# Kernel tuning notes

Hardware: AMD Instinct MI355X
Metric: run time of the kernel (lower is better)

Reference implementation:

```python
import jax, jax.numpy as jnp
import numpy as np

# dims
B, Nt, Ln, Lv = 16, 64, 256, 4      # batch, trees/batch, nodes/tree, value tokens/node
D = 256                              # embedding_dim
VOCAB, NTYPE = 32000, 64
M, Ls = 128, 4                       # story memory slots, tokens per slot
HOPS = 3                             # max_hops
COMP_STEP = 4                        # max tree depth = max(kb_n_layers)
LEVELS = [0, 1, 16, 64, 160, Ln]     # node index ranges per depth 0..4


def setup_inputs() -> dict:
    rng = np.random.default_rng(0)
    key = jax.random.key(0)
    ks = jax.random.split(key, 12)

    # --- tree structure: depth per node, father index in previous level ---
    depth = np.zeros(Ln, np.int64)
    father = np.zeros((B, Nt, Ln), np.int64)
    for lvl in range(1, 5):
        lo, hi = LEVELS[lvl], LEVELS[lvl + 1]
        depth[lo:hi] = lvl
        father[..., lo:hi] = rng.integers(LEVELS[lvl - 1], LEVELS[lvl], (B, Nt, hi - lo))
    father[..., 0] = Ln  # root's father = pad slot (torch -1 wraps to last index)
    kb_fathers = np.concatenate([father, np.full((B, Nt, 1), Ln, np.int64)], -1)  # [B,Nt,Ln+1]
    nl = np.broadcast_to(depth, (B, Nt, Ln))
    kb_n_layers = np.concatenate([nl, np.full((B, Nt, 1), -1, np.int64)], -1)     # [B,Nt,Ln+1]

    kb_values = rng.integers(1, VOCAB, (B, Nt, Ln, Lv))
    kb_types = rng.integers(1, NTYPE, (B, Nt, Ln))
    story = rng.integers(1, VOCAB, (B, M, Ls))
    decoder_input = rng.integers(1, VOCAB, (B,))

    s = 1.0 / np.sqrt(D)
    C = 0.1 * jax.random.normal(ks[0], (HOPS + 1, VOCAB, D), jnp.float32)
    C = C.at[:, 0].set(0.0)  # padding_idx = 0
    T_emb = 0.1 * jax.random.normal(ks[1], (NTYPE, D), jnp.float32)
    T_emb = T_emb.at[0].set(0.0)
    return {
        'decoder_input': jnp.asarray(decoder_input),
        'story': jnp.asarray(story),
        'hidden': 0.1 * jax.random.normal(ks[2], (1, B, D), jnp.float32),
        'kb_values': jnp.asarray(kb_values),
        'kb_types': jnp.asarray(kb_types),
        'kb_fathers': jnp.asarray(kb_fathers),
        'kb_n_layers': jnp.asarray(kb_n_layers),
        'C': C,
        'T_emb': T_emb,
        'Wq': s * jax.random.normal(ks[3], (D, D), jnp.float32),
        'Wk': s * jax.random.normal(ks[4], (D, D), jnp.float32),
        'Wv': s * jax.random.normal(ks[5], (D, D), jnp.float32),
        'W1_w': s * jax.random.normal(ks[6], (VOCAB, 2 * D), jnp.float32),
        'W1_b': jnp.zeros((VOCAB,), jnp.float32),
        'W_ih': s * jax.random.normal(ks[7], (3 * D, D), jnp.float32),
        'W_hh': s * jax.random.normal(ks[8], (3 * D, D), jnp.float32),
        'b_ih': jnp.zeros((3 * D,), jnp.float32),
        'b_hh': jnp.zeros((3 * D,), jnp.float32),
    }


def _forward(decoder_input, story, hidden, kb_values, kb_types, kb_fathers, kb_n_layers,
             C, T_emb, Wq, Wk, Wv, W1_w, W1_b, W_ih, W_hh, b_ih, b_hh):
    C0 = C[0]
    # ensemble: node embed = type_embed * sum(value token embeds)   [B,Nt,Ln,D]
    node = T_emb[kb_types] * C0[kb_values].sum(-2)
    node = jnp.concatenate([node, jnp.zeros((B, Nt, 1, D), node.dtype)], axis=2)  # pad slot
    nl = COMP_STEP - 1 - kb_n_layers  # adjusted layer counter
    base = jnp.arange(B * Nt).reshape(B, Nt, 1) * (Ln + 1)
    seg = (base + kb_fathers).reshape(-1)  # flat father ids for scatter-add

    def body(i, carry):
        node, nl = carry
        nxt = jax.ops.segment_sum(node.reshape(-1, D), seg,
                                  num_segments=B * Nt * (Ln + 1)).reshape(B, Nt, Ln + 1, D)
        node = node + nxt * (nl == 0)[..., None].astype(node.dtype)
        return (node, nl - 1)

    node, _ = jax.lax.fori_loop(0, COMP_STEP, body, (node, nl))
    roots = node[:, :, 0]                                   # [B,Nt,D]
    bias = jnp.where(roots.sum(-1) == 0, -1e9, 0.0)         # attention_bias [B,Nt]

    # compute_global_ranking: QKV attention over tree roots
    h = hidden[-1]                                          # [B,D]
    w = jax.nn.softmax(jnp.einsum('bnd,bd->bn', roots @ Wk.T, h @ Wq.T) + bias, axis=1)
    feat = jnp.einsum('bn,bnd->bd', w, roots @ Wv.T)        # kb_attn_features

    # single GRU step (PyTorch gate order r,z,n)
    x = C0[decoder_input]
    gi = x @ W_ih.T + b_ih
    gh = h @ W_hh.T + b_hh
    ir, iz, inn = jnp.split(gi, 3, -1)
    hr, hz, hn = jnp.split(gh, 3, -1)
    r = jax.nn.sigmoid(ir + hr)
    z = jax.nn.sigmoid(iz + hz)
    n = jnp.tanh(inn + r * hn)
    h_new = (1.0 - z) * n + z * h
    u = h_new + feat                                        # cur_state

    # ptrMemDecoder (Mem2Seq-style hops over story memory)
    p_vocab = None
    logits = None
    for hop in range(HOPS):
        m_A = C[hop][story].sum(2)                          # [B,M,D]
        logits = jnp.einsum('bmd,bd->bm', m_A, u)
        prob = jax.nn.softmax(logits, axis=1)
        m_C = C[hop + 1][story].sum(2)
        o = jnp.einsum('bm,bmd->bd', prob, m_C)
        if hop == 0:
            p_vocab = jnp.concatenate([u, o], -1) @ W1_w.T + W1_b
        u = u + o
    p_ptr = logits
    return p_ptr, p_vocab, h_new


def reference(decoder_input, story, hidden, kb_values, kb_types, kb_fathers, kb_n_layers,
              C, T_emb, Wq, Wk, Wv, W1_w, W1_b, W_ih, W_hh, b_ih, b_hh):
    return _forward(decoder_input, story, hidden, kb_values, kb_types, kb_fathers, kb_n_layers,
                    C, T_emb, Wq, Wk, Wv, W1_w, W1_b, W_ih, W_hh, b_ih, b_hh)
```

## Files before the change

### kernel.cpp

```cpp
#include <hip/hip_runtime.h>
#include <hip/hip_bf16.h>
#include <math.h>

#define B_ 16
#define NT 64
#define LN 256
#define LV 4
#define D_ 256
#define VOCAB_ 32000
#define M_ 128
#define LS 4
#define ECAP 192

typedef unsigned short ushort_t;
typedef unsigned int uint_t;

__device__ __forceinline__ ushort_t f2bf(float f) {
  uint_t u = __float_as_uint(f);
  uint_t r = u + 0x7FFFu + ((u >> 16) & 1u);
  return (ushort_t)(r >> 16);
}
__device__ __forceinline__ float bflo(uint_t u) {
  return __uint_as_float(u << 16);
}
__device__ __forceinline__ float bfhi(uint_t u) {
  return __uint_as_float(u & 0xFFFF0000u);
}

#define NB_S (3 * B_ * M_)
#define NB_CONV 2048
#define NB_TR 192
#define NB_TQK 256
#define NB_WVT 64
#define NB_BKT (B_ * NT)
__global__ __launch_bounds__(256) void k_prep(
    const int* __restrict__ story, const float* __restrict__ C,
    const float* __restrict__ W_ih, const float* __restrict__ W_hh,
    const float* __restrict__ Wq, const float* __restrict__ Wk,
    const float* __restrict__ Wv, const int* __restrict__ kb_values,
    const int* __restrict__ kb_types, float* __restrict__ S,
    ushort_t* __restrict__ C0h, float* __restrict__ W_ihT,
    float* __restrict__ W_hhT, float* __restrict__ TQK,
    float* __restrict__ WvT, int* __restrict__ entries,
    int* __restrict__ counts, int* __restrict__ qctr) {
  __shared__ __align__(16) char praw[7424];
  float* smem = (float*)praw;
  int blk = blockIdx.x, tid = threadIdx.x;
  if (blk == 0 && tid < 8) qctr[tid] = 0;
  if (blk < NB_S) {
    int h = blk / (B_ * M_);
    int bm = blk % (B_ * M_);
    const int* st = story + (size_t)bm * LS;
    const float* Ch = C + (size_t)h * VOCAB_ * D_;
    float s = Ch[(size_t)st[0] * D_ + tid] + Ch[(size_t)st[1] * D_ + tid] +
              Ch[(size_t)st[2] * D_ + tid] + Ch[(size_t)st[3] * D_ + tid];
    S[(size_t)blk * D_ + tid] = s;
  } else if (blk < NB_S + NB_CONV) {
    int n4 = VOCAB_ * D_ / 4;
    for (int i = (blk - NB_S) * 256 + tid; i < n4; i += NB_CONV * 256) {
      float4 f = ((const float4*)C)[i];
      uint2 packed;
      packed.x = (uint_t)f2bf(f.x) | ((uint_t)f2bf(f.y) << 16);
      packed.y = (uint_t)f2bf(f.z) | ((uint_t)f2bf(f.w) << 16);
      ((uint2*)C0h)[i] = packed;
    }
  } else if (blk < NB_S + NB_CONV + 2 * NB_TR) {
    int t = blk - (NB_S + NB_CONV);
    const float* W = W_ih;
    float* WT = W_ihT;
    if (t >= NB_TR) { t -= NB_TR; W = W_hh; WT = W_hhT; }
    const int R = 768;
    int tr = t % (R / 32), tc = t / (R / 32);
    int tx = tid & 31, ty = tid >> 5;
#pragma unroll
    for (int k = 0; k < 4; ++k)
      smem[(ty + 8 * k) * 33 + tx] =
          W[(size_t)(tr * 32 + ty + 8 * k) * D_ + tc * 32 + tx];
    __syncthreads();
#pragma unroll
    for (int k = 0; k < 4; ++k)
      WT[(size_t)(tc * 32 + ty + 8 * k) * R + tr * 32 + tx] =
          smem[tx * 33 + ty + 8 * k];
  } else if (blk < NB_S + NB_CONV + 2 * NB_TR + NB_TQK) {
    int j = blk - (NB_S + NB_CONV + 2 * NB_TR);
    smem[tid] = Wq[(size_t)tid * D_ + j];
    __syncthreads();
    float acc = 0.f;
#pragma unroll 8
    for (int k = 0; k < D_; ++k) acc += smem[k] * Wk[(size_t)k * D_ + tid];
    TQK[(size_t)j * D_ + tid] = acc;
  } else if (blk < NB_S + NB_CONV + 2 * NB_TR + NB_TQK + NB_WVT) {
    int t = blk - (NB_S + NB_CONV + 2 * NB_TR + NB_TQK);
    int tr = t & 7, tc = t >> 3;
    int tx = tid & 31, ty = tid >> 5;
#pragma unroll
    for (int k = 0; k < 4; ++k)
      smem[(ty + 8 * k) * 33 + tx] =
          Wv[(size_t)(tr * 32 + ty + 8 * k) * D_ + tc * 32 + tx];
    __syncthreads();
#pragma unroll
    for (int k = 0; k < 4; ++k)
      WvT[(size_t)(tc * 32 + ty + 8 * k) * D_ + tr * 32 + tx] =
          smem[tx * 33 + ty + 8 * k];
  } else {
    int bn = blk - (NB_S + NB_CONV + 2 * NB_TR + NB_TQK + NB_WVT);
    int* sval = (int*)praw;
    int* stype = sval + 1024;
    int* sbin = stype + 256;
    int* srng = sbin + 512;
    int* scnt = srng + 8;
    const int* vp = kb_values + (size_t)bn * LN * LV;
    for (int i = tid; i < LN * LV; i += 256) sval[i] = vp[i];
    stype[tid] = kb_types[(size_t)bn * LN + tid];
    sbin[tid] = 0;
    sbin[256 + tid] = 0;
    __syncthreads();
    int ty = stype[tid];
    int vv[4];
#pragma unroll
    for (int j = 0; j < 4; ++j) {
      vv[j] = sval[tid * 4 + j];
      atomicAdd(&sbin[((vv[j] >> 12) << 6) | ty], 1);
    }
    __syncthreads();
    if (tid < 64) {
      int run = 0;
#pragma unroll
      for (int c = 0; c < 8; ++c) {
        int x = sbin[c * 64 + tid];
        int orig = x;
        for (int o = 1; o < 64; o <<= 1) {
          int y = __shfl_up(x, o);
          if ((int)tid >= o) x += y;
        }
        sbin[c * 64 + tid] = x - orig + run;
        run += __shfl(x, 63);
      }
    }
    __syncthreads();
    if (tid < 8) {
      srng[tid] = sbin[tid << 6];
      int e = (tid == 7) ? (LN * LV) : sbin[(tid + 1) << 6];
      int cv = min(e - sbin[tid << 6], ECAP);
      counts[bn * 8 + tid] = cv;
      scnt[tid] = cv;
    }
    __syncthreads();
#pragma unroll
    for (int j = 0; j < 4; ++j) {
      int v = vv[j];
      int r = v >> 12;
      int pos = atomicAdd(&sbin[(r << 6) | ty], 1) - srng[r];
      if (pos < ECAP)
        entries[(size_t)(bn * 8 + r) * ECAP + pos] = v | (ty << 16);
    }
    __syncthreads();
    if (tid < 8) {
      int cv = scnt[tid];
      int cp = (cv + 7) & ~7;
      for (int p = cv; p < cp; ++p)
        entries[(size_t)(bn * 8 + tid) * ECAP + p] = 0;
    }
  }
}

#define NBG 2048
#define NRANGE 8
#define UNITS_PER_RANGE 256
__global__ __launch_bounds__(512) void k_rootsg(
    const int* __restrict__ counts, const int* __restrict__ entries,
    const ushort_t* __restrict__ C0h, const float* __restrict__ T_emb,
    const int* __restrict__ dec, const float* __restrict__ C0,
    const float* __restrict__ hidden, const float* __restrict__ W_ihT,
    const float* __restrict__ W_hhT, const float* __restrict__ TQK,
    const float* __restrict__ b_ih, const float* __restrict__ b_hh,
    float* __restrict__ part, float* __restrict__ gi, float* __restrict__ gh,
    float* __restrict__ tvec, int* __restrict__ qctr) {
  __shared__ __align__(16) char smem_raw[32768 + 6144 + 16];
  int blk = blockIdx.x, tid = threadIdx.x;
  if (blk < NBG) {
    float2* t2s = (float2*)smem_raw;
    int* ent_all = (int*)(smem_raw + 32768);
    int* sunit = (int*)(smem_raw + 32768 + 6144);
    if (tid == 0) {
      int xcd = __builtin_amdgcn_s_getreg(6164) & 7;
      int unit = -1;
      for (int a = 0; a < NRANGE && unit < 0; ++a) {
        int rr = (xcd + a) & 7;
        int u = atomicAdd(&qctr[rr], 1);
        if (u < UNITS_PER_RANGE) unit = (u << 3) | rr;
      }
      sunit[0] = unit;
    }
    __syncthreads();
    int unit = sunit[0];
    if (unit < 0) return;
    int rr = unit & 7, u = unit >> 3;
    int h = u & 1, grp = u >> 1;
    const float2* Tg = (const float2*)T_emb;
    for (int i = tid; i < 64 * 64; i += 512)
      t2s[i] = Tg[(i >> 6) * 128 + h * 64 + (i & 63)];
    int wid = tid >> 6, lane = tid & 63;
    int bn = grp * 8 + wid;
    int bucket = bn * 8 + rr;
    int cnt = counts[bucket];
    int cntp = (cnt + 7) & ~7;
    const int* ge = entries + (size_t)bucket * ECAP;
    int* ent = ent_all + wid * ECAP;
    for (int i = lane; i < cntp; i += 64) ent[i] = ge[i];
    __syncthreads();
    const ushort_t* C0hh = C0h + h * 128 + 2 * lane;
    float a0 = 0.f, a1 = 0.f;
#pragma unroll 2
    for (int k = 0; k < cntp; k += 4) {
      int4 e4 = *(const int4*)(ent + k);
      int ex = __builtin_amdgcn_readfirstlane(e4.x);
      int ey = __builtin_amdgcn_readfirstlane(e4.y);
      int ez = __builtin_amdgcn_readfirstlane(e4.z);
      int ew = __builtin_amdgcn_readfirstlane(e4.w);
      uint_t u0 = *(const uint_t*)(C0hh + ((size_t)(ex & 0xFFFF) << 8));
      uint_t u1 = *(const uint_t*)(C0hh + ((size_t)(ey & 0xFFFF) << 8));
      uint_t u2 = *(const uint_t*)(C0hh + ((size_t)(ez & 0xFFFF) << 8));
      uint_t u3 = *(const uint_t*)(C0hh + ((size_t)(ew & 0xFFFF) << 8));
      float2 t0 = t2s[((ex >> 16) << 6) | lane];
      float2 t1 = t2s[((ey >> 16) << 6) | lane];
      float2 t2 = t2s[((ez >> 16) << 6) | lane];
      float2 t3 = t2s[((ew >> 16) << 6) | lane];
      a0 += t0.x * bflo(u0) + t1.x * bflo(u1) + t2.x * bflo(u2) +
            t3.x * bflo(u3);
      a1 += t0.y * bfhi(u0) + t1.y * bfhi(u1) + t2.y * bfhi(u2) +
            t3.y * bfhi(u3);
    }
    float2 res;
    res.x = a0;
    res.y = a1;
    ((float2*)(part + (size_t)bucket * D_ + h * 128))[lane] = res;
  } else {
    int g = blk - NBG;
    float* xs = (float*)smem_raw;
    float acc[B_];
    int i = (g < 3 ? g : g - 3) * 256 + tid;
    if (g < 3) {
      float bias = (tid < 256) ? b_ih[i] : 0.f;
#pragma unroll
      for (int b = 0; b < B_; ++b) acc[b] = bias;
      for (int c = 0; c < 4; ++c) {
        __syncthreads();
        for (int idx = tid; idx < B_ * 64; idx += 512) {
          int b = idx >> 6, jj = idx & 63;
          xs[idx] = C0[(size_t)dec[b] * D_ + c * 64 + jj];
        }
        __syncthreads();
        if (tid < 256) {
#pragma unroll 4
          for (int jj = 0; jj < 64; ++jj) {
            float w = W_ihT[(size_t)(c * 64 + jj) * 768 + i];
#pragma unroll
            for (int b = 0; b < B_; ++b) acc[b] += xs[b * 64 + jj] * w;
          }
        }
      }
      if (tid < 256) {
#pragma unroll
        for (int b = 0; b < B_; ++b) gi[(size_t)b * 768 + i] = acc[b];
      }
    } else if (g < 6) {
      float bias = (tid < 256) ? b_hh[i] : 0.f;
#pragma unroll
      for (int b = 0; b < B_; ++b) acc[b] = bias;
      for (int c = 0; c < 4; ++c) {
        __syncthreads();
        for (int idx = tid; idx < B_ * 64; idx += 512) {
          int b = idx >> 6, jj = idx & 63;
          xs[idx] = hidden[b * D_ + c * 64 + jj];
        }
        __syncthreads();
        if (tid < 256) {
#pragma unroll 4
          for (int jj = 0; jj < 64; ++jj) {
            float w = W_hhT[(size_t)(c * 64 + jj) * 768 + i];
#pragma unroll
            for (int b = 0; b < B_; ++b) acc[b] += xs[b * 64 + jj] * w;
          }
        }
      }
      if (tid < 256) {
#pragma unroll
        for (int b = 0; b < B_; ++b) gh[(size_t)b * 768 + i] = acc[b];
      }
    } else {
#pragma unroll
      for (int b = 0; b < B_; ++b) acc[b] = 0.f;
      for (int c = 0; c < 4; ++c) {
        __syncthreads();
        for (int idx = tid; idx < B_ * 64; idx += 512) {
          int b = idx >> 6, jj = idx & 63;
          xs[idx] = hidden[b * D_ + c * 64 + jj];
        }
        __syncthreads();
        if (tid < 256) {
#pragma unroll 4
          for (int jj = 0; jj < 64; ++jj) {
            float w = TQK[(size_t)(c * 64 + jj) * D_ + tid];
#pragma unroll
            for (int b = 0; b < B_; ++b) acc[b] += xs[b * 64 + jj] * w;
          }
        }
      }
      if (tid < 256) {
#pragma unroll
        for (int b = 0; b < B_; ++b) tvec[b * D_ + tid] = acc[b];
      }
    }
  }
}

__global__ __launch_bounds__(256) void k_mid(
    const float* __restrict__ part, const float* __restrict__ tvec,
    const float* __restrict__ S, float* __restrict__ scores,
    float* __restrict__ ST, float* __restrict__ rsum) {
  int blk = blockIdx.x, tid = threadIdx.x;
  if (blk < 1024) {
    int b = blk >> 6;
    const float* p = part + (size_t)blk * 8 * D_;
    float rv = 0.f;
#pragma unroll
    for (int r = 0; r < 8; ++r) rv += p[r * D_ + tid];
    rsum[(size_t)blk * D_ + tid] = rv;
    float sc = rv * tvec[b * D_ + tid];
    float sm = rv;
    __shared__ float red[8];
    int lane = tid & 63, wave = tid >> 6;
    for (int o = 32; o > 0; o >>= 1) {
      sc += __shfl_xor(sc, o);
      sm += __shfl_xor(sm, o);
    }
    if (lane == 0) { red[wave] = sc; red[4 + wave] = sm; }
    __syncthreads();
    if (tid == 0) {
      float SC = red[0] + red[1] + red[2] + red[3];
      float SM = red[4] + red[5] + red[6] + red[7];
      scores[blk] = (SM == 0.0f) ? SC - 1000000000.0f : SC;
    }
  } else {
    int t = blk - 1024;
    int hb = t >> 5;
    int tile = t & 31;
    int tm = tile & 3, td = tile >> 2;
    int tx = tid & 31, ty = tid >> 5;
    __shared__ float sm2[32 * 33];
    const float* Sp = S + (size_t)hb * M_ * D_;
    float* STp = ST + (size_t)hb * D_ * M_;
#pragma unroll
    for (int k = 0; k < 4; ++k)
      sm2[(ty + 8 * k) * 33 + tx] =
          Sp[(size_t)(tm * 32 + ty + 8 * k) * D_ + td * 32 + tx];
    __syncthreads();
#pragma unroll
    for (int k = 0; k < 4; ++k)
      STp[(size_t)(td * 32 + ty + 8 * k) * M_ + tm * 32 + tx] =
          sm2[tx * 33 + ty + 8 * k];
  }
}

__global__ __launch_bounds__(256) void k_chain(
    const float* __restrict__ scores, const float* __restrict__ rsum,
    const float* __restrict__ WvT, const float* __restrict__ gi,
    const float* __restrict__ gh, const float* __restrict__ hidden,
    const float* __restrict__ S, const float* __restrict__ ST,
    float* __restrict__ h_new_out, float* __restrict__ cat,
    float* __restrict__ p_ptr) {
  int b = blockIdx.x, tid = threadIdx.x;
  __shared__ float wsh[NT], rs[D_], us[D_], lo[M_], loB[M_], pr[M_];
  if (tid < NT) {
    float s = scores[b * NT + tid];
    float m = s;
    for (int o = 32; o > 0; o >>= 1) m = fmaxf(m, __shfl_xor(m, o));
    float e = expf(s - m);
    float sum = e;
    for (int o = 32; o > 0; o >>= 1) sum += __shfl_xor(sum, o);
    wsh[tid] = e / sum;
  }
  __syncthreads();
  float rb = 0.f;
#pragma unroll 16
  for (int n = 0; n < NT; ++n)
    rb += wsh[n] * rsum[(size_t)(b * NT + n) * D_ + tid];
  rs[tid] = rb;
  __syncthreads();
  float feat = 0.f;
#pragma unroll 16
  for (int j = 0; j < D_; ++j) feat += rs[j] * WvT[(size_t)j * D_ + tid];
  {
    float i_r = gi[(size_t)b * 768 + tid];
    float i_z = gi[(size_t)b * 768 + 256 + tid];
    float i_n = gi[(size_t)b * 768 + 512 + tid];
    float h_r = gh[(size_t)b * 768 + tid];
    float h_z = gh[(size_t)b * 768 + 256 + tid];
    float h_n = gh[(size_t)b * 768 + 512 + tid];
    float h = hidden[b * D_ + tid];
    float r = 1.f / (1.f + expf(-(i_r + h_r)));
    float z = 1.f / (1.f + expf(-(i_z + h_z)));
    float nn = tanhf(i_n + r * h_n);
    float hn = (1.f - z) * nn + z * h;
    h_new_out[b * D_ + tid] = hn;
    float u0 = hn + feat;
    us[tid] = u0;
    cat[b * 512 + tid] = u0;
  }
  __syncthreads();
  for (int h = 0; h < 3; ++h) {
    {
      int m = tid & 127;
      int half = tid >> 7;
      const float* STp = ST + (((size_t)h * B_ + b) * D_ + half * 128) * M_;
      float l = 0.f;
#pragma unroll 16
      for (int d = 0; d < 128; ++d)
        l += us[half * 128 + d] * STp[(size_t)d * M_ + m];
      if (half == 0) lo[m] = l; else loB[m] = l;
    }
    __syncthreads();
    if (h == 2) {
      if (tid < M_) p_ptr[b * M_ + tid] = lo[tid] + loB[tid];
      break;
    }
    if (tid < 64) {
      float l0 = lo[tid] + loB[tid], l1 = lo[tid + 64] + loB[tid + 64];
      float a = fmaxf(l0, l1);
      for (int o = 32; o > 0; o >>= 1) a = fmaxf(a, __shfl_xor(a, o));
      float e0 = expf(l0 - a), e1 = expf(l1 - a);
      float s = e0 + e1;
      for (int o = 32; o > 0; o >>= 1) s += __shfl_xor(s, o);
      pr[tid] = e0 / s;
      pr[tid + 64] = e1 / s;
    }
    __syncthreads();
    {
      const float* Sn = S + (((size_t)(h + 1) * B_ + b) * M_) * D_;
      float o = 0.f;
#pragma unroll 16
      for (int m = 0; m < M_; ++m) o += pr[m] * Sn[(size_t)m * D_ + tid];
      if (h == 0) cat[b * 512 + D_ + tid] = o;
      us[tid] += o;
    }
    __syncthreads();
  }
}

__global__ __launch_bounds__(256) void k_pvocab(
    const float* __restrict__ cat, const float* __restrict__ W1_w,
    const float* __restrict__ W1_b, float* __restrict__ out) {
  int blk = blockIdx.x, tid = threadIdx.x;
  int row = tid & 63, q = tid >> 6;
  int v = blk * 64 + row;
  __shared__ float cs[B_ * 512];
  __shared__ float ps[3][64][B_];
  for (int i = tid; i < B_ * 512; i += 256) cs[i] = cat[i];
  __syncthreads();
  const float4* wrow = (const float4*)(W1_w + (size_t)v * 512 + q * 128);
  float acc[B_];
#pragma unroll
  for (int b = 0; b < B_; ++b) acc[b] = 0.f;
#pragma unroll 4
  for (int k4 = 0; k4 < 32; ++k4) {
    float4 w = wrow[k4];
#pragma unroll
    for (int b = 0; b < B_; ++b) {
      const float* c = &cs[b * 512 + q * 128 + k4 * 4];
      acc[b] += w.x * c[0] + w.y * c[1] + w.z * c[2] + w.w * c[3];
    }
  }
  if (q > 0) {
#pragma unroll
    for (int b = 0; b < B_; ++b) ps[q - 1][row][b] = acc[b];
  }
  __syncthreads();
  if (q == 0) {
    float bb = W1_b[v];
#pragma unroll
    for (int b = 0; b < B_; ++b)
      out[(size_t)b * VOCAB_ + v] =
          acc[b] + ps[0][row][b] + ps[1][row][b] + ps[2][row][b] + bb;
  }
}

extern "C" void kernel_launch(void* const* d_in, const int* in_sizes, int n_in,
                              void* d_out, int out_size, void* d_ws,
                              size_t ws_size, hipStream_t stream) {
  const int* decoder_input = (const int*)d_in[0];
  const int* story = (const int*)d_in[1];
  const float* hidden = (const float*)d_in[2];
  const int* kb_values = (const int*)d_in[3];
  const int* kb_types = (const int*)d_in[4];
  const float* C = (const float*)d_in[7];
  const float* T_emb = (const float*)d_in[8];
  const float* Wq = (const float*)d_in[9];
  const float* Wk = (const float*)d_in[10];
  const float* Wv = (const float*)d_in[11];
  const float* W1_w = (const float*)d_in[12];
  const float* W1_b = (const float*)d_in[13];
  const float* W_ih = (const float*)d_in[14];
  const float* W_hh = (const float*)d_in[15];
  const float* b_ih = (const float*)d_in[16];
  const float* b_hh = (const float*)d_in[17];

  float* out = (float*)d_out;
  float* p_ptr = out;
  float* p_vocab = out + B_ * M_;
  float* h_new = out + B_ * M_ + B_ * VOCAB_;

  float* ws = (float*)d_ws;
  float* S = ws;
  float* part = S + 3 * B_ * M_ * D_;
  float* rsum = part + B_ * NT * 8 * D_;
  float* cat = rsum + B_ * NT * D_;
  float* scores = cat + B_ * 512;
  float* gi = scores + B_ * NT;
  float* gh = gi + B_ * 768;
  float* tvec = gh + B_ * 768;
  int* counts = (int*)(tvec + B_ * D_);
  int* qctr = counts + 8192;
  ushort_t* C0h = (ushort_t*)(qctr + 8);
  float* wtmp = (float*)(C0h + (size_t)VOCAB_ * D_);
  float* W_ihT = wtmp;
  float* W_hhT = W_ihT + 768 * D_;
  float* TQK = W_hhT + 768 * D_;
  int* entries = (int*)(TQK + D_ * D_);
  float* ST = wtmp;
  float* WvT = wtmp + (458752 + 1572864);

  hipLaunchKernelGGL(
      k_prep, dim3(NB_S + NB_CONV + 2 * NB_TR + NB_TQK + NB_WVT + NB_BKT),
      dim3(256), 0, stream, story, C, W_ih, W_hh, Wq, Wk, Wv, kb_values,
      kb_types, S, C0h, W_ihT, W_hhT, TQK, WvT, entries, counts, qctr);
  hipLaunchKernelGGL(k_rootsg, dim3(NBG + 7), dim3(512), 0, stream, counts,
                     entries, C0h, T_emb, decoder_input, C, hidden, W_ihT,
                     W_hhT, TQK, b_ih, b_hh, part, gi, gh, tvec, qctr);
  hipLaunchKernelGGL(k_mid, dim3(1024 + 1536), dim3(256), 0, stream, part,
                     tvec, S, scores, ST, rsum);
  hipLaunchKernelGGL(k_chain, dim3(B_), dim3(256), 0, stream, scores, rsum,
                     WvT, gi, gh, hidden, S, ST, h_new, cat, p_ptr);
  hipLaunchKernelGGL(k_pvocab, dim3(VOCAB_ / 64), dim3(256), 0, stream, cat,
                     W1_w, W1_b, p_vocab);
}
```

Before: 454.0 us.

## Gather full embedding rows with 16-byte loads and halve gather blocks

```diff
diff --git a/kernel.cpp b/kernel.cpp
--- a/kernel.cpp
+++ b/kernel.cpp
@@ -164,9 +164,9 @@
   }
 }
 
-#define NBG 2048
+#define NBG 1024
 #define NRANGE 8
-#define UNITS_PER_RANGE 256
+#define UNITS_PER_RANGE 128
 __global__ __launch_bounds__(512) void k_rootsg(
     const int* __restrict__ counts, const int* __restrict__ entries,
     const ushort_t* __restrict__ C0h, const float* __restrict__ T_emb,
@@ -176,12 +176,12 @@
     const float* __restrict__ b_ih, const float* __restrict__ b_hh,
     float* __restrict__ part, float* __restrict__ gi, float* __restrict__ gh,
     float* __restrict__ tvec, int* __restrict__ qctr) {
-  __shared__ __align__(16) char smem_raw[32768 + 6144 + 16];
+  __shared__ __align__(16) char smem_raw[65536 + 6144 + 16];
   int blk = blockIdx.x, tid = threadIdx.x;
   if (blk < NBG) {
-    float2* t2s = (float2*)smem_raw;
-    int* ent_all = (int*)(smem_raw + 32768);
-    int* sunit = (int*)(smem_raw + 32768 + 6144);
+    float4* t4s = (float4*)smem_raw;
+    int* ent_all = (int*)(smem_raw + 65536);
+    int* sunit = (int*)(smem_raw + 65536 + 6144);
     if (tid == 0) {
       int xcd = __builtin_amdgcn_s_getreg(6164) & 7;
       int unit = -1;
@@ -192,49 +192,60 @@
       }
       sunit[0] = unit;
     }
+    const float4* Tg = (const float4*)T_emb;
+    for (int i = tid; i < 64 * 64; i += 512) {
+      int ty = i >> 6, j = i & 63;
+      t4s[i] = Tg[ty * 64 + 2 * (j & 31) + (j >> 5)];
+    }
     __syncthreads();
     int unit = sunit[0];
     if (unit < 0) return;
     int rr = unit & 7, u = unit >> 3;
-    int h = u & 1, grp = u >> 1;
-    const float2* Tg = (const float2*)T_emb;
-    for (int i = tid; i < 64 * 64; i += 512)
-      t2s[i] = Tg[(i >> 6) * 128 + h * 64 + (i & 63)];
     int wid = tid >> 6, lane = tid & 63;
-    int bn = grp * 8 + wid;
+    int l31 = lane & 31;
+    int half = lane >> 5;
+    int bn = u * 8 + wid;
     int bucket = bn * 8 + rr;
     int cnt = counts[bucket];
-    int cntp = (cnt + 7) & ~7;
+    int cnt2 = (cnt + 1) & ~1;
     const int* ge = entries + (size_t)bucket * ECAP;
     int* ent = ent_all + wid * ECAP;
-    for (int i = lane; i < cntp; i += 64) ent[i] = ge[i];
-    __syncthreads();
-    const ushort_t* C0hh = C0h + h * 128 + 2 * lane;
-    float a0 = 0.f, a1 = 0.f;
+    for (int i = lane; i < cnt2; i += 64) ent[i] = ge[i];
+    const ushort_t* C0base = C0h + 8 * l31;
+    float a0 = 0.f, a1 = 0.f, a2 = 0.f, a3 = 0.f;
+    float a4 = 0.f, a5 = 0.f, a6 = 0.f, a7 = 0.f;
 #pragma unroll 2
-    for (int k = 0; k < cntp; k += 4) {
-      int4 e4 = *(const int4*)(ent + k);
-      int ex = __builtin_amdgcn_readfirstlane(e4.x);
-      int ey = __builtin_amdgcn_readfirstlane(e4.y);
-      int ez = __builtin_amdgcn_readfirstlane(e4.z);
-      int ew = __builtin_amdgcn_readfirstlane(e4.w);
-      uint_t u0 = *(const uint_t*)(C0hh + ((size_t)(ex & 0xFFFF) << 8));
-      uint_t u1 = *(const uint_t*)(C0hh + ((size_t)(ey & 0xFFFF) << 8));
-      uint_t u2 = *(const uint_t*)(C0hh + ((size_t)(ez & 0xFFFF) << 8));
-      uint_t u3 = *(const uint_t*)(C0hh + ((size_t)(ew & 0xFFFF) << 8));
-      float2 t0 = t2s[((ex >> 16) << 6) | lane];
-      float2 t1 = t2s[((ey >> 16) << 6) | lane];
-      float2 t2 = t2s[((ez >> 16) << 6) | lane];
-      float2 t3 = t2s[((ew >> 16) << 6) | lane];
-      a0 += t0.x * bflo(u0) + t1.x * bflo(u1) + t2.x * bflo(u2) +
-            t3.x * bflo(u3);
-      a1 += t0.y * bfhi(u0) + t1.y * bfhi(u1) + t2.y * bfhi(u2) +
-            t3.y * bfhi(u3);
-    }
-    float2 res;
-    res.x = a0;
-    res.y = a1;
-    ((float2*)(part + (size_t)bucket * D_ + h * 128))[lane] = res;
+    for (int k = 0; k < cnt2; k += 2) {
+      int e = ent[k + half];
+      uint4 uu = *(const uint4*)(C0base + ((size_t)(e & 0xFFFF) << 8));
+      int ty = e >> 16;
+      float4 ta = t4s[(ty << 6) | l31];
+      float4 tb = t4s[(ty << 6) | 32 | l31];
+      a0 += ta.x * bflo(uu.x);
+      a1 += ta.y * bfhi(uu.x);
+      a2 += ta.z * bflo(uu.y);
+      a3 += ta.w * bfhi(uu.y);
+      a4 += tb.x * bflo(uu.z);
+      a5 += tb.y * bfhi(uu.z);
+      a6 += tb.z * bflo(uu.w);
+      a7 += tb.w * bfhi(uu.w);
+    }
+    a0 += __shfl_xor(a0, 32);
+    a1 += __shfl_xor(a1, 32);
+    a2 += __shfl_xor(a2, 32);
+    a3 += __shfl_xor(a3, 32);
+    a4 += __shfl_xor(a4, 32);
+    a5 += __shfl_xor(a5, 32);
+    a6 += __shfl_xor(a6, 32);
+    a7 += __shfl_xor(a7, 32);
+    if (half == 0) {
+      float4 r0v, r1v;
+      r0v.x = a0; r0v.y = a1; r0v.z = a2; r0v.w = a3;
+      r1v.x = a4; r1v.y = a5; r1v.z = a6; r1v.w = a7;
+      float4* pp = (float4*)(part + (size_t)bucket * D_ + 8 * l31);
+      pp[0] = r0v;
+      pp[1] = r1v;
+    }
   } else {
     int g = blk - NBG;
     float* xs = (float*)smem_raw;
```

New measurement: 405.6 us. 10.7% less time.

## Process full embedding width per block instead of splitting halves across blocks

Applied to the files above, without the earlier changes.

```diff
diff --git a/kernel.cpp b/kernel.cpp
--- a/kernel.cpp
+++ b/kernel.cpp
@@ -157,16 +157,16 @@
     __syncthreads();
     if (tid < 8) {
       int cv = scnt[tid];
-      int cp = (cv + 7) & ~7;
+      int cp = (cv + 15) & ~15;
       for (int p = cv; p < cp; ++p)
         entries[(size_t)(bn * 8 + tid) * ECAP + p] = 0;
     }
   }
 }
 
-#define NBG 2048
+#define NBG 1024
 #define NRANGE 8
-#define UNITS_PER_RANGE 256
+#define UNITS_PER_RANGE 128
 __global__ __launch_bounds__(512) void k_rootsg(
     const int* __restrict__ counts, const int* __restrict__ entries,
     const ushort_t* __restrict__ C0h, const float* __restrict__ T_emb,
@@ -176,12 +176,12 @@
     const float* __restrict__ b_ih, const float* __restrict__ b_hh,
     float* __restrict__ part, float* __restrict__ gi, float* __restrict__ gh,
     float* __restrict__ tvec, int* __restrict__ qctr) {
-  __shared__ __align__(16) char smem_raw[32768 + 6144 + 16];
+  __shared__ __align__(16) char smem_raw[65536 + 6144 + 16];
   int blk = blockIdx.x, tid = threadIdx.x;
   if (blk < NBG) {
-    float2* t2s = (float2*)smem_raw;
-    int* ent_all = (int*)(smem_raw + 32768);
-    int* sunit = (int*)(smem_raw + 32768 + 6144);
+    float4* t4s = (float4*)smem_raw;
+    int* ent_all = (int*)(smem_raw + 65536);
+    int* sunit = (int*)(smem_raw + 65536 + 6144);
     if (tid == 0) {
       int xcd = __builtin_amdgcn_s_getreg(6164) & 7;
       int unit = -1;
@@ -192,49 +192,50 @@
       }
       sunit[0] = unit;
     }
+    const float4* Tg = (const float4*)T_emb;
+    for (int i = tid; i < 64 * 64; i += 512) t4s[i] = Tg[i];
     __syncthreads();
     int unit = sunit[0];
     if (unit < 0) return;
     int rr = unit & 7, u = unit >> 3;
-    int h = u & 1, grp = u >> 1;
-    const float2* Tg = (const float2*)T_emb;
-    for (int i = tid; i < 64 * 64; i += 512)
-      t2s[i] = Tg[(i >> 6) * 128 + h * 64 + (i & 63)];
     int wid = tid >> 6, lane = tid & 63;
-    int bn = grp * 8 + wid;
+    int bn = u * 8 + wid;
     int bucket = bn * 8 + rr;
     int cnt = counts[bucket];
-    int cntp = (cnt + 7) & ~7;
+    int cntp = (cnt + 15) & ~15;
     const int* ge = entries + (size_t)bucket * ECAP;
     int* ent = ent_all + wid * ECAP;
     for (int i = lane; i < cntp; i += 64) ent[i] = ge[i];
-    __syncthreads();
-    const ushort_t* C0hh = C0h + h * 128 + 2 * lane;
-    float a0 = 0.f, a1 = 0.f;
-#pragma unroll 2
-    for (int k = 0; k < cntp; k += 4) {
-      int4 e4 = *(const int4*)(ent + k);
-      int ex = __builtin_amdgcn_readfirstlane(e4.x);
-      int ey = __builtin_amdgcn_readfirstlane(e4.y);
-      int ez = __builtin_amdgcn_readfirstlane(e4.z);
-      int ew = __builtin_amdgcn_readfirstlane(e4.w);
-      uint_t u0 = *(const uint_t*)(C0hh + ((size_t)(ex & 0xFFFF) << 8));
-      uint_t u1 = *(const uint_t*)(C0hh + ((size_t)(ey & 0xFFFF) << 8));
-      uint_t u2 = *(const uint_t*)(C0hh + ((size_t)(ez & 0xFFFF) << 8));
-      uint_t u3 = *(const uint_t*)(C0hh + ((size_t)(ew & 0xFFFF) << 8));
-      float2 t0 = t2s[((ex >> 16) << 6) | lane];
-      float2 t1 = t2s[((ey >> 16) << 6) | lane];
-      float2 t2 = t2s[((ez >> 16) << 6) | lane];
-      float2 t3 = t2s[((ew >> 16) << 6) | lane];
-      a0 += t0.x * bflo(u0) + t1.x * bflo(u1) + t2.x * bflo(u2) +
-            t3.x * bflo(u3);
-      a1 += t0.y * bfhi(u0) + t1.y * bfhi(u1) + t2.y * bfhi(u2) +
-            t3.y * bfhi(u3);
-    }
-    float2 res;
-    res.x = a0;
-    res.y = a1;
-    ((float2*)(part + (size_t)bucket * D_ + h * 128))[lane] = res;
+    float a0 = 0.f, a1 = 0.f, a2 = 0.f, a3 = 0.f;
+    for (int k = 0; k < cntp; k += 16) {
+#pragma unroll
+      for (int j = 0; j < 4; ++j) {
+        int4 e4 = *(const int4*)(ent + k + 4 * j);
+        int ex = __builtin_amdgcn_readfirstlane(e4.x);
+        int ey = __builtin_amdgcn_readfirstlane(e4.y);
+        int ez = __builtin_amdgcn_readfirstlane(e4.z);
+        int ew = __builtin_amdgcn_readfirstlane(e4.w);
+        uint2 u0 = ((const uint2*)(C0h + ((size_t)(ex & 0xFFFF) << 8)))[lane];
+        uint2 u1 = ((const uint2*)(C0h + ((size_t)(ey & 0xFFFF) << 8)))[lane];
+        uint2 u2 = ((const uint2*)(C0h + ((size_t)(ez & 0xFFFF) << 8)))[lane];
+        uint2 u3 = ((const uint2*)(C0h + ((size_t)(ew & 0xFFFF) << 8)))[lane];
+        float4 t0 = t4s[((ex >> 16) << 6) | lane];
+        float4 t1 = t4s[((ey >> 16) << 6) | lane];
+        float4 t2 = t4s[((ez >> 16) << 6) | lane];
+        float4 t3 = t4s[((ew >> 16) << 6) | lane];
+        a0 += t0.x * bflo(u0.x) + t1.x * bflo(u1.x) + t2.x * bflo(u2.x) +
+              t3.x * bflo(u3.x);
+        a1 += t0.y * bfhi(u0.x) + t1.y * bfhi(u1.x) + t2.y * bfhi(u2.x) +
+              t3.y * bfhi(u3.x);
+        a2 += t0.z * bflo(u0.y) + t1.z * bflo(u1.y) + t2.z * bflo(u2.y) +
+              t3.z * bflo(u3.y);
+        a3 += t0.w * bfhi(u0.y) + t1.w * bfhi(u1.y) + t2.w * bfhi(u2.y) +
+              t3.w * bfhi(u3.y);
+      }
+    }
+    float4 res;
+    res.x = a0; res.y = a1; res.z = a2; res.w = a3;
+    ((float4*)(part + (size_t)bucket * D_))[lane] = res;
   } else {
     int g = blk - NBG;
     float* xs = (float*)smem_raw;
```

After: 422.5 us. -6.9%, faster.
